# Kernel tuning notes

Hardware: AMD Instinct MI355X
Metric: run time of the kernel (lower is better)

## Reference

```python
import jax, jax.numpy as jnp
import numpy as np

NUM_HEADS = 4
HIDDEN = 128
LN_EPS = 1e-6
NEG_INF = -1e9


def setup_inputs() -> dict:
    key = jax.random.key(0)
    ks = jax.random.split(key, 8)
    B, S, H, NH = 64, 512, HIDDEN, NUM_HEADS
    enc = jax.random.normal(ks[0], (B, S, H), dtype=jnp.float32)
    mask = jax.random.randint(ks[1], (B, 1, S, S), 0, 2, dtype=jnp.int32)
    scale = 1.0 / np.sqrt(H)
    # torch Linear(H, H*NH, bias=False): weight is (H*NH, H); store transposed (H, H*NH)
    Wq = jax.random.normal(ks[2], (H, H * NH), dtype=jnp.float32) * scale
    Wk = jax.random.normal(ks[3], (H, H * NH), dtype=jnp.float32) * scale
    Wv = jax.random.normal(ks[4], (H, H * NH), dtype=jnp.float32) * scale
    Wo = jax.random.normal(ks[5], (H * NH, H), dtype=jnp.float32) * (1.0 / np.sqrt(H * NH))
    gamma = jnp.ones((H,), dtype=jnp.float32)
    beta = jnp.zeros((H,), dtype=jnp.float32)
    return {"enc": enc, "mask": mask, "Wq": Wq, "Wk": Wk, "Wv": Wv, "Wo": Wo, "gamma": gamma, "beta": beta}


def reference(enc, mask, Wq, Wk, Wv, Wo, gamma, beta):
    B, S, H = enc.shape
    NH = NUM_HEADS
    # projections -> (B, NH, S, H): each head has head_dim == hidden_units
    Q = (enc @ Wq).reshape(B, S, NH, H).transpose(0, 2, 1, 3)
    K = (enc @ Wk).reshape(B, S, NH, H).transpose(0, 2, 1, 3)
    V = (enc @ Wv).reshape(B, S, NH, H).transpose(0, 2, 1, 3)
    # scaled dot-product attention with mask (non-flash: full score matrix)
    scores = jnp.einsum('bhqd,bhkd->bhqk', Q, K) / jnp.sqrt(jnp.float32(H))
    scores = jnp.where(mask == 0, jnp.float32(NEG_INF), scores)
    attn = jax.nn.softmax(scores, axis=-1)  # dropout = identity in eval mode
    ctx = jnp.einsum('bhqk,bhkd->bhqd', attn, V)  # (B, NH, S, H)
    ctx = ctx.transpose(0, 2, 1, 3).reshape(B, S, NH * H)
    out = ctx @ Wo + enc  # dropout identity, residual add
    # LayerNorm over last dim
    mu = jnp.mean(out, axis=-1, keepdims=True)
    var = jnp.var(out, axis=-1, keepdims=True)
    return gamma * (out - mu) / jnp.sqrt(var + LN_EPS) + beta
```

## Files before the change

### kernel.cpp

```cpp
#include <hip/hip_runtime.h>
#include <stdint.h>

#define BATCH 64
#define SLEN 512
#define HID 128
#define NHEAD 4
#define DPROJ 512
#define MTOT (BATCH * SLEN)
#define SCALE 0.08838834764831845f

using short8 = __attribute__((ext_vector_type(8))) short;
using f32x4  = __attribute__((ext_vector_type(4))) float;
using u32x4  = __attribute__((ext_vector_type(4))) unsigned int;
using u32x2  = __attribute__((ext_vector_type(2))) unsigned int;
using us4    = __attribute__((ext_vector_type(4))) unsigned short;

__device__ __forceinline__ unsigned short f2bf(float f) {
  unsigned int u = __float_as_uint(f);
  u += 0x7fffu + ((u >> 16) & 1u);
  return (unsigned short)(u >> 16);
}

__global__ __launch_bounds__(256) void prep_kernel(
    const float* __restrict__ Wq,
    const float* __restrict__ Wk,
    const float* __restrict__ Wv,
    const float* __restrict__ Wo,
    const float* __restrict__ enc,
    unsigned short* __restrict__ WT,
    unsigned short* __restrict__ WoT,
    unsigned short* __restrict__ encb)
{
  if (blockIdx.x < 1024) {
    int idx = blockIdx.x * 256 + threadIdx.x;
    int z = idx >> 16;
    int i = idx & 65535;
    if (z < 3) {
      const float* W = (z == 0) ? Wq : (z == 1) ? Wk : Wv;
      float scale = (z == 0) ? SCALE : 1.0f;
      int k = i >> 9;
      int n = i & 511;
      WT[(size_t)z * 65536 + (size_t)n * 128 + k] = f2bf(W[i] * scale);
    } else {
      int k = i >> 7;
      int n = i & 127;
      WoT[(size_t)n * 512 + k] = f2bf(Wo[i]);
    }
  } else {
    size_t tid = (size_t)(blockIdx.x - 1024) * 256 + threadIdx.x;
    const float* s = enc + tid * 8;
    f32x4 a0 = *(const f32x4*)(s);
    f32x4 a1 = *(const f32x4*)(s + 4);
    short8 v;
    #pragma unroll
    for (int j = 0; j < 4; ++j) v[j] = (short)f2bf(a0[j]);
    #pragma unroll
    for (int j = 0; j < 4; ++j) v[4 + j] = (short)f2bf(a1[j]);
    *(short8*)(encb + tid * 8) = v;
  }
}

__global__ __launch_bounds__(256) void maskpack_kernel(
    const int* __restrict__ mask,
    unsigned int* __restrict__ mbits)
{
  size_t idx = (size_t)blockIdx.x * 256 + threadIdx.x;
  int m = mask[idx];
  unsigned long long bal = __ballot(m != 0);
  if ((threadIdx.x & 63) == 0)
    *(unsigned long long*)(mbits + (idx >> 5)) = bal;
}

__global__ __launch_bounds__(256) void qkv_kernel(
    const unsigned short* __restrict__ encb,
    const unsigned short* __restrict__ WT,
    unsigned short* __restrict__ Qh,
    unsigned short* __restrict__ Kh,
    unsigned short* __restrict__ Vt)
{
  const int nt = blockIdx.x;
  const int mt = blockIdx.y;
  const int t = threadIdx.x;
  const int lane = t & 63;
  const int w = t >> 6;
  const int quad = lane >> 4;
  const int l16 = lane & 15;

  __shared__ __align__(16) unsigned short Ald[128 * 136];
  __shared__ __align__(16) unsigned short Bld[128 * 136];

  const int m0 = mt * 128, n0 = nt * 128;
  const int wm = (w >> 1) * 64, wn = (w & 1) * 64;

  #pragma unroll
  for (int i = 0; i < 8; ++i) {
    int idx = i * 256 + t;
    int row = idx >> 4;
    int col = (idx & 15) << 3;
    *(u32x4*)(Ald + row * 136 + col) =
        *(const u32x4*)(encb + (size_t)(m0 + row) * HID + col);
  }

  for (int z = 0; z < 3; ++z) {
    __syncthreads();
    const unsigned short* Wz = WT + (size_t)z * DPROJ * HID;
    #pragma unroll
    for (int i = 0; i < 8; ++i) {
      int idx = i * 256 + t;
      int row = idx >> 4;
      int col = (idx & 15) << 3;
      *(u32x4*)(Bld + row * 136 + col) =
          *(const u32x4*)(Wz + (size_t)(n0 + row) * HID + col);
    }
    __syncthreads();

    f32x4 acc[4][4];
    #pragma unroll
    for (int mi = 0; mi < 4; ++mi)
      #pragma unroll
      for (int ni = 0; ni < 4; ++ni)
        acc[mi][ni] = f32x4{0.f, 0.f, 0.f, 0.f};

    #pragma unroll
    for (int kk = 0; kk < 4; ++kk) {
      short8 a[4], bb[4];
      #pragma unroll
      for (int mi = 0; mi < 4; ++mi)
        a[mi] = *(const short8*)(Ald + (wm + mi * 16 + l16) * 136 + kk * 32 + quad * 8);
      #pragma unroll
      for (int ni = 0; ni < 4; ++ni)
        bb[ni] = *(const short8*)(Bld + (wn + ni * 16 + l16) * 136 + kk * 32 + quad * 8);
      if (z < 2) {
        #pragma unroll
        for (int mi = 0; mi < 4; ++mi)
          #pragma unroll
          for (int ni = 0; ni < 4; ++ni)
            acc[mi][ni] = __builtin_amdgcn_mfma_f32_16x16x32_bf16(bb[ni], a[mi], acc[mi][ni], 0, 0, 0);
      } else {
        #pragma unroll
        for (int mi = 0; mi < 4; ++mi)
          #pragma unroll
          for (int ni = 0; ni < 4; ++ni)
            acc[mi][ni] = __builtin_amdgcn_mfma_f32_16x16x32_bf16(a[mi], bb[ni], acc[mi][ni], 0, 0, 0);
      }
    }

    if (z < 2) {
      unsigned short* outz = ((z == 0) ? Qh : Kh) + (size_t)nt * MTOT * HID;
      #pragma unroll
      for (int mi = 0; mi < 4; ++mi)
        #pragma unroll
        for (int ni = 0; ni < 4; ++ni) {
          int m = m0 + wm + mi * 16 + l16;
          int dbase = wn + ni * 16 + quad * 4;
          us4 pk;
          #pragma unroll
          for (int r = 0; r < 4; ++r) pk[r] = f2bf(acc[mi][ni][r]);
          *(us4*)(outz + (size_t)m * HID + dbase) = pk;
        }
    } else {
      #pragma unroll
      for (int mi = 0; mi < 4; ++mi)
        #pragma unroll
        for (int ni = 0; ni < 4; ++ni) {
          int row0 = m0 + wm + mi * 16 + quad * 4;
          int b = row0 >> 9, s = row0 & 511;
          int d = wn + ni * 16 + l16;
          us4 pk;
          #pragma unroll
          for (int r = 0; r < 4; ++r) pk[r] = f2bf(acc[mi][ni][r]);
          *(us4*)(Vt + ((size_t)(nt * BATCH + b) * HID + d) * SLEN + s) = pk;
        }
    }
  }
}

__global__ __launch_bounds__(512, 4) void attn_kernel(
    const unsigned short* __restrict__ Qh,
    const unsigned short* __restrict__ Kh,
    const unsigned short* __restrict__ Vt,
    const unsigned int* __restrict__ mbits,
    unsigned short* __restrict__ ctx)
{
  const int lin = blockIdx.x;
  const int work = (lin & 7) * 128 + (lin >> 3);
  const int qt = work & 3;
  const int h  = (work >> 2) & 3;
  const int b  = work >> 4;

  const int t = threadIdx.x;
  const int lane = t & 63;
  const int w = t >> 6;
  const int quad = lane >> 4;
  const int l16 = lane & 15;

  __shared__ __align__(16) unsigned short Kld[64 * 136];
  __shared__ __align__(16) unsigned short Vtld[128 * 72];
  __shared__ __align__(16) unsigned short Pld[128 * 72];

  const int q0 = qt * 128;
  const size_t rowbase = (size_t)b * SLEN;
  const unsigned short* kbase0 = Kh + ((size_t)h * MTOT + rowbase) * HID;
  const unsigned short* vbase  = Vt + (size_t)(h * BATCH + b) * HID * SLEN;
  const unsigned int* mrow = mbits + (size_t)b * SLEN * 16;

  const int k_key = t >> 4,           k_col = (t & 15) << 3;
  const int v_d   = t >> 3,           v_cc  = (t & 7) << 3;

  short8 qa[4];
  {
    const unsigned short* qbase =
        Qh + ((size_t)h * MTOT + rowbase + q0 + w * 16 + l16) * HID + quad * 8;
    #pragma unroll
    for (int kk = 0; kk < 4; ++kk)
      qa[kk] = *(const short8*)(qbase + kk * 32);
  }

  short8 ones;
  #pragma unroll
  for (int j = 0; j < 8; ++j) ones[j] = (short)0x3F80;

  f32x4 oc[8], oc9;
  #pragma unroll
  for (int nd = 0; nd < 8; ++nd) oc[nd] = f32x4{0.f, 0.f, 0.f, 0.f};
  oc9 = f32x4{0.f, 0.f, 0.f, 0.f};

  u32x4 kreg[2], vreg[2];
  #pragma unroll
  for (int i = 0; i < 2; ++i) {
    kreg[i] = *(const u32x4*)(kbase0 + (size_t)(k_key + i * 32) * HID + k_col);
    vreg[i] = *(const u32x4*)(vbase + (size_t)(v_d + i * 64) * SLEN + v_cc);
  }

  for (int c0 = 0; c0 < SLEN; c0 += 64) {
    if (c0) __syncthreads();
    #pragma unroll
    for (int i = 0; i < 2; ++i) {
      *(u32x4*)(Kld + (k_key + i * 32) * 136 + k_col) = kreg[i];
      *(u32x4*)(Vtld + (v_d + i * 64) * 72 + v_cc) = vreg[i];
    }
    __syncthreads();
    if (c0 + 64 < SLEN) {
      #pragma unroll
      for (int i = 0; i < 2; ++i) {
        kreg[i] = *(const u32x4*)(kbase0 + (size_t)(c0 + 64 + k_key + i * 32) * HID + k_col);
        vreg[i] = *(const u32x4*)(vbase + (size_t)(v_d + i * 64) * SLEN + c0 + 64 + v_cc);
      }
    }

    u32x2 mw[4];
    #pragma unroll
    for (int r = 0; r < 4; ++r) {
      int qrow = q0 + w * 16 + quad * 4 + r;
      mw[r] = *(const u32x2*)(mrow + (size_t)qrow * 16 + (c0 >> 5));
    }

    f32x4 sc[4];
    #pragma unroll
    for (int ni = 0; ni < 4; ++ni) sc[ni] = f32x4{0.f, 0.f, 0.f, 0.f};
    #pragma unroll
    for (int kk = 0; kk < 4; ++kk) {
      #pragma unroll
      for (int ni = 0; ni < 4; ++ni) {
        short8 bb = *(const short8*)(Kld + (ni * 16 + l16) * 136 + kk * 32 + quad * 8);
        sc[ni] = __builtin_amdgcn_mfma_f32_16x16x32_bf16(qa[kk], bb, sc[ni], 0, 0, 0);
      }
    }

    #pragma unroll
    for (int ni = 0; ni < 4; ++ni) {
      int bit = (ni & 1) * 16 + l16;
      #pragma unroll
      for (int r = 0; r < 4; ++r) {
        unsigned wsel = (ni < 2) ? mw[r][0] : mw[r][1];
        float e = __expf(sc[ni][r]);
        float p = ((wsel >> bit) & 1u) ? e : 0.f;
        Pld[(w * 16 + quad * 4 + r) * 72 + ni * 16 + l16] = f2bf(p);
      }
    }
    __threadfence_block();

    #pragma unroll
    for (int kb = 0; kb < 2; ++kb) {
      short8 a = *(const short8*)(Pld + (w * 16 + l16) * 72 + kb * 32 + quad * 8);
      #pragma unroll
      for (int nd = 0; nd < 8; ++nd) {
        short8 bv = *(const short8*)(Vtld + (nd * 16 + l16) * 72 + kb * 32 + quad * 8);
        oc[nd] = __builtin_amdgcn_mfma_f32_16x16x32_bf16(a, bv, oc[nd], 0, 0, 0);
      }
      oc9 = __builtin_amdgcn_mfma_f32_16x16x32_bf16(a, ones, oc9, 0, 0, 0);
    }
  }

  #pragma unroll
  for (int nd = 0; nd < 8; ++nd)
    #pragma unroll
    for (int r = 0; r < 4; ++r) {
      float val = oc[nd][r] / oc9[r];
      int row = q0 + w * 16 + quad * 4 + r;
      int col = h * HID + nd * 16 + l16;
      ctx[(rowbase + row) * DPROJ + col] = f2bf(val);
    }
}

__global__ __launch_bounds__(256, 4) void oproj_ln_kernel(
    const unsigned short* __restrict__ ctx,
    const unsigned short* __restrict__ WoT,
    const float* __restrict__ enc,
    const float* __restrict__ gamma,
    const float* __restrict__ beta,
    float* __restrict__ out)
{
  const int m0 = blockIdx.x * 64;
  const int t = threadIdx.x;
  const int lane = t & 63;
  const int w = t >> 6;
  const int quad = lane >> 4;
  const int l16 = lane & 15;

  __shared__ __align__(16) unsigned short Actx[64 * 72];
  __shared__ __align__(16) unsigned short Bw[128 * 72];

  f32x4 acc[8];
  #pragma unroll
  for (int ni = 0; ni < 8; ++ni) acc[ni] = f32x4{0.f, 0.f, 0.f, 0.f};

  for (int kc = 0; kc < DPROJ; kc += 64) {
    __syncthreads();
    #pragma unroll
    for (int i = 0; i < 2; ++i) {
      int idx = i * 256 + t;
      int row = idx >> 3;
      int col = (idx & 7) << 3;
      *(u32x4*)(Actx + row * 72 + col) =
          *(const u32x4*)(ctx + (size_t)(m0 + row) * DPROJ + kc + col);
    }
    #pragma unroll
    for (int i = 0; i < 4; ++i) {
      int idx = i * 256 + t;
      int row = idx >> 3;
      int col = (idx & 7) << 3;
      *(u32x4*)(Bw + row * 72 + col) =
          *(const u32x4*)(WoT + (size_t)row * DPROJ + kc + col);
    }
    __syncthreads();
    #pragma unroll
    for (int kk = 0; kk < 2; ++kk) {
      short8 a = *(const short8*)(Actx + (w * 16 + l16) * 72 + kk * 32 + quad * 8);
      #pragma unroll
      for (int ni = 0; ni < 8; ++ni) {
        short8 bb = *(const short8*)(Bw + (ni * 16 + l16) * 72 + kk * 32 + quad * 8);
        acc[ni] = __builtin_amdgcn_mfma_f32_16x16x32_bf16(a, bb, acc[ni], 0, 0, 0);
      }
    }
  }

  float g[8], be[8];
  #pragma unroll
  for (int ni = 0; ni < 8; ++ni) {
    g[ni] = gamma[ni * 16 + l16];
    be[ni] = beta[ni * 16 + l16];
  }

  float val[8][4];
  #pragma unroll
  for (int r = 0; r < 4; ++r) {
    int m = m0 + w * 16 + quad * 4 + r;
    const float* erow = enc + (size_t)m * HID;
    float s = 0.f, s2 = 0.f;
    #pragma unroll
    for (int ni = 0; ni < 8; ++ni) {
      float v = acc[ni][r] + erow[ni * 16 + l16];
      val[ni][r] = v;
      s += v;
      s2 += v * v;
    }
    #pragma unroll
    for (int off = 1; off < 16; off <<= 1) {
      s  += __shfl_xor(s, off, 64);
      s2 += __shfl_xor(s2, off, 64);
    }
    float mean = s * (1.f / 128.f);
    float var = s2 * (1.f / 128.f) - mean * mean;
    float rstd = rsqrtf(var + 1e-6f);
    float* orow = out + (size_t)m * HID;
    #pragma unroll
    for (int ni = 0; ni < 8; ++ni)
      orow[ni * 16 + l16] = g[ni] * (val[ni][r] - mean) * rstd + be[ni];
  }
}

extern "C" void kernel_launch(void* const* d_in, const int* in_sizes, int n_in,
                              void* d_out, int out_size, void* d_ws, size_t ws_size,
                              hipStream_t stream) {
  const float* enc   = (const float*)d_in[0];
  const int*   mask  = (const int*)d_in[1];
  const float* Wq    = (const float*)d_in[2];
  const float* Wk    = (const float*)d_in[3];
  const float* Wv    = (const float*)d_in[4];
  const float* Wo    = (const float*)d_in[5];
  const float* gamma = (const float*)d_in[6];
  const float* beta  = (const float*)d_in[7];
  float* out = (float*)d_out;

  unsigned short* WT  = (unsigned short*)d_ws;
  unsigned short* WoT = WT + (size_t)3 * DPROJ * HID;
  unsigned short* Qh  = WoT + (size_t)HID * DPROJ;
  unsigned short* Kh  = Qh + (size_t)NHEAD * MTOT * HID;
  unsigned short* Vt  = Kh + (size_t)NHEAD * MTOT * HID;
  unsigned short* ctx = Vt + (size_t)NHEAD * MTOT * HID;
  unsigned short* encb = ctx + (size_t)MTOT * DPROJ;
  unsigned int* mbits = (unsigned int*)(encb + (size_t)MTOT * HID * 2);

  prep_kernel<<<3072, 256, 0, stream>>>(Wq, Wk, Wv, Wo, enc, WT, WoT, encb);
  maskpack_kernel<<<65536, 256, 0, stream>>>(mask, mbits);
  qkv_kernel<<<dim3(4, 256), 256, 0, stream>>>(encb, WT, Qh, Kh, Vt);
  attn_kernel<<<1024, 512, 0, stream>>>(Qh, Kh, Vt, mbits, ctx);
  oproj_ln_kernel<<<MTOT / 64, 256, 0, stream>>>(ctx, WoT, enc, gamma, beta, out);
}
```

Measured before the change: 256.0 us.

## Fuse mask packing into prep kernel, swizzle P tile, transpose PV MFMA output

Merges the mask bit-packing kernel into the prep kernel, giving each wave four ballots instead of one. This saves a launch and uses fewer, larger blocks. In attention, the P tile in LDS switches from a padded layout to an XOR-swizzled unpadded one to cut bank conflicts and LDS footprint. The PV MFMA operands are swapped so each lane holds four contiguous output columns of one query row. That allows a single reciprocal and packed 8-byte ctx stores instead of scattered 2-byte stores with per-element division.

Result: faster. 246.5 us (-3.7%).

```diff
diff --git a/kernel.cpp b/kernel.cpp
--- a/kernel.cpp
+++ b/kernel.cpp
@@ -27,9 +27,11 @@
     const float* __restrict__ Wv,
     const float* __restrict__ Wo,
     const float* __restrict__ enc,
+    const int* __restrict__ mask,
     unsigned short* __restrict__ WT,
     unsigned short* __restrict__ WoT,
-    unsigned short* __restrict__ encb)
+    unsigned short* __restrict__ encb,
+    unsigned int* __restrict__ mbits)
 {
   if (blockIdx.x < 1024) {
     int idx = blockIdx.x * 256 + threadIdx.x;
@@ -46,7 +48,7 @@
       int n = i & 127;
       WoT[(size_t)n * 512 + k] = f2bf(Wo[i]);
     }
-  } else {
+  } else if (blockIdx.x < 3072) {
     size_t tid = (size_t)(blockIdx.x - 1024) * 256 + threadIdx.x;
     const float* s = enc + tid * 8;
     f32x4 a0 = *(const f32x4*)(s);
@@ -57,18 +59,18 @@
     #pragma unroll
     for (int j = 0; j < 4; ++j) v[4 + j] = (short)f2bf(a1[j]);
     *(short8*)(encb + tid * 8) = v;
-  }
-}
-
-__global__ __launch_bounds__(256) void maskpack_kernel(
-    const int* __restrict__ mask,
-    unsigned int* __restrict__ mbits)
-{
-  size_t idx = (size_t)blockIdx.x * 256 + threadIdx.x;
-  int m = mask[idx];
-  unsigned long long bal = __ballot(m != 0);
-  if ((threadIdx.x & 63) == 0)
-    *(unsigned long long*)(mbits + (idx >> 5)) = bal;
+  } else {
+    const int l = threadIdx.x & 63;
+    size_t wavebase = (size_t)(blockIdx.x - 3072) * 1024 + (threadIdx.x >> 6) * 256;
+    unsigned long long b0 = __ballot(mask[wavebase + 0 * 64 + l] != 0);
+    unsigned long long b1 = __ballot(mask[wavebase + 1 * 64 + l] != 0);
+    unsigned long long b2 = __ballot(mask[wavebase + 2 * 64 + l] != 0);
+    unsigned long long b3 = __ballot(mask[wavebase + 3 * 64 + l] != 0);
+    if (l < 4) {
+      unsigned long long v = (l & 2) ? ((l & 1) ? b3 : b2) : ((l & 1) ? b1 : b0);
+      *(unsigned long long*)(mbits + (wavebase >> 5) + l * 2) = v;
+    }
+  }
 }
 
 __global__ __launch_bounds__(256) void qkv_kernel(
@@ -196,7 +198,7 @@
 
   __shared__ __align__(16) unsigned short Kld[64 * 136];
   __shared__ __align__(16) unsigned short Vtld[128 * 72];
-  __shared__ __align__(16) unsigned short Pld[128 * 72];
+  __shared__ __align__(16) unsigned short Pld[128 * 64];
 
   const int q0 = qt * 128;
   const size_t rowbase = (size_t)b * SLEN;
@@ -204,8 +206,8 @@
   const unsigned short* vbase  = Vt + (size_t)(h * BATCH + b) * HID * SLEN;
   const unsigned int* mrow = mbits + (size_t)b * SLEN * 16;
 
-  const int k_key = t >> 4,           k_col = (t & 15) << 3;
-  const int v_d   = t >> 3,           v_cc  = (t & 7) << 3;
+  const int k_key = t >> 4, k_col = (t & 15) << 3;
+  const int v_d   = t >> 3, v_cc  = (t & 7) << 3;
 
   short8 qa[4];
   {
@@ -275,32 +277,37 @@
         unsigned wsel = (ni < 2) ? mw[r][0] : mw[r][1];
         float e = __expf(sc[ni][r]);
         float p = ((wsel >> bit) & 1u) ? e : 0.f;
-        Pld[(w * 16 + quad * 4 + r) * 72 + ni * 16 + l16] = f2bf(p);
+        int rowp = w * 16 + quad * 4 + r;
+        int cg = (ni * 2 + (l16 >> 3)) ^ (rowp & 7);
+        Pld[rowp * 64 + cg * 8 + (l16 & 7)] = f2bf(p);
       }
     }
     __threadfence_block();
 
     #pragma unroll
     for (int kb = 0; kb < 2; ++kb) {
-      short8 a = *(const short8*)(Pld + (w * 16 + l16) * 72 + kb * 32 + quad * 8);
+      int rowr = w * 16 + l16;
+      int cg = (kb * 4 + quad) ^ (l16 & 7);
+      short8 a = *(const short8*)(Pld + rowr * 64 + cg * 8);
       #pragma unroll
       for (int nd = 0; nd < 8; ++nd) {
         short8 bv = *(const short8*)(Vtld + (nd * 16 + l16) * 72 + kb * 32 + quad * 8);
-        oc[nd] = __builtin_amdgcn_mfma_f32_16x16x32_bf16(a, bv, oc[nd], 0, 0, 0);
-      }
-      oc9 = __builtin_amdgcn_mfma_f32_16x16x32_bf16(a, ones, oc9, 0, 0, 0);
-    }
-  }
-
-  #pragma unroll
-  for (int nd = 0; nd < 8; ++nd)
-    #pragma unroll
-    for (int r = 0; r < 4; ++r) {
-      float val = oc[nd][r] / oc9[r];
-      int row = q0 + w * 16 + quad * 4 + r;
-      int col = h * HID + nd * 16 + l16;
-      ctx[(rowbase + row) * DPROJ + col] = f2bf(val);
-    }
+        oc[nd] = __builtin_amdgcn_mfma_f32_16x16x32_bf16(bv, a, oc[nd], 0, 0, 0);
+      }
+      oc9 = __builtin_amdgcn_mfma_f32_16x16x32_bf16(ones, a, oc9, 0, 0, 0);
+    }
+  }
+
+  float rcp = 1.0f / oc9[0];
+  int qrow = q0 + w * 16 + l16;
+  unsigned short* crow = ctx + (rowbase + qrow) * DPROJ + h * HID;
+  #pragma unroll
+  for (int nd = 0; nd < 8; ++nd) {
+    us4 pk;
+    #pragma unroll
+    for (int r = 0; r < 4; ++r) pk[r] = f2bf(oc[nd][r] * rcp);
+    *(us4*)(crow + nd * 16 + quad * 4) = pk;
+  }
 }
 
 __global__ __launch_bounds__(256, 4) void oproj_ln_kernel(
@@ -412,8 +419,7 @@
   unsigned short* encb = ctx + (size_t)MTOT * DPROJ;
   unsigned int* mbits = (unsigned int*)(encb + (size_t)MTOT * HID * 2);
 
-  prep_kernel<<<3072, 256, 0, stream>>>(Wq, Wk, Wv, Wo, enc, WT, WoT, encb);
-  maskpack_kernel<<<65536, 256, 0, stream>>>(mask, mbits);
+  prep_kernel<<<19456, 256, 0, stream>>>(Wq, Wk, Wv, Wo, enc, mask, WT, WoT, encb, mbits);
   qkv_kernel<<<dim3(4, 256), 256, 0, stream>>>(encb, WT, Qh, Kh, Vt);
   attn_kernel<<<1024, 512, 0, stream>>>(Qh, Kh, Vt, mbits, ctx);
   oproj_ln_kernel<<<MTOT / 64, 256, 0, stream>>>(ctx, WoT, enc, gamma, beta, out);
```
